# Kernel tuning notes

Hardware: AMD Instinct MI355X
Metric: run time of the kernel (lower is better)

## Reference

```python
import jax, jax.numpy as jnp
import numpy as np

N, E, H, L, T, NH = 20000, 200000, 128, 10, 2, 4


def _ln(x, g, b, eps=1e-5):
    mu = jnp.mean(x, -1, keepdims=True)
    d = x - mu
    v = jnp.mean(d * d, -1, keepdims=True)
    return d * jax.lax.rsqrt(v + eps) * g + b


def _mha(q_in, kv_in, wqkv, bqkv, wo, bo, nh=NH):
    # torch nn.MultiheadAttention (batch=1, eval mode)
    Hd = q_in.shape[-1]
    d = Hd // nh
    wq, wk, wv = jnp.split(wqkv, 3, axis=1)
    bq, bk, bv = jnp.split(bqkv, 3)
    q = (q_in @ wq + bq).reshape(-1, nh, d)
    k = (kv_in @ wk + bk).reshape(-1, nh, d)
    v = (kv_in @ wv + bv).reshape(-1, nh, d)
    s = jnp.einsum('qhd,khd->hqk', q, k) / jnp.sqrt(jnp.float32(d))
    a = jax.nn.softmax(s, axis=-1)
    o = jnp.einsum('hqk,khd->qhd', a, v).reshape(-1, Hd)
    return o @ wo + bo


def setup_inputs() -> dict:
    key = jax.random.key(0)
    ks = iter(jax.random.split(key, 64))
    def rn(shape, scale=1.0):
        return jax.random.normal(next(ks), shape, jnp.float32) * scale
    s = 0.05
    inp = {}
    inp['x'] = rn((N, H))
    inp['edge_index'] = jax.random.randint(next(ks), (2, E), 0, N)
    inp['edge_attr'] = rn((E, H))
    # per-layer edge MLP: Linear(3H,2H) LN GELU Linear(2H,H) LN
    inp['edge_w1'] = rn((L, 3 * H, 2 * H), s); inp['edge_b1'] = jnp.zeros((L, 2 * H))
    inp['edge_ln1g'] = jnp.ones((L, 2 * H)); inp['edge_ln1b'] = jnp.zeros((L, 2 * H))
    inp['edge_w2'] = rn((L, 2 * H, H), s); inp['edge_b2'] = jnp.zeros((L, H))
    inp['edge_ln2g'] = jnp.ones((L, H)); inp['edge_ln2b'] = jnp.zeros((L, H))
    # per-layer node MLP: Linear(3H,2H) LN GELU Linear(2H,H) LN
    inp['node_w1'] = rn((L, 3 * H, 2 * H), s); inp['node_b1'] = jnp.zeros((L, 2 * H))
    inp['node_ln1g'] = jnp.ones((L, 2 * H)); inp['node_ln1b'] = jnp.zeros((L, 2 * H))
    inp['node_w2'] = rn((L, 2 * H, H), s); inp['node_b2'] = jnp.zeros((L, H))
    inp['node_ln2g'] = jnp.ones((L, H)); inp['node_ln2b'] = jnp.zeros((L, H))
    # GlobalTokenTransformer (shared across layers)
    inp['token_embed'] = rn((T, H), 0.02)
    inp['tok_wqkv'] = rn((H, 3 * H), s); inp['tok_bqkv'] = jnp.zeros(3 * H)
    inp['tok_wo'] = rn((H, H), s); inp['tok_bo'] = jnp.zeros(H)
    inp['ln_t1g'] = jnp.ones(H); inp['ln_t1b'] = jnp.zeros(H)
    inp['ln_t2g'] = jnp.ones(H); inp['ln_t2b'] = jnp.zeros(H)
    inp['ff_w1'] = rn((H, 4 * H), s); inp['ff_b1'] = jnp.zeros(4 * H)
    inp['ff_w2'] = rn((4 * H, H), s); inp['ff_b2'] = jnp.zeros(H)
    inp['nod_wqkv'] = rn((H, 3 * H), s); inp['nod_bqkv'] = jnp.zeros(3 * H)
    inp['nod_wo'] = rn((H, H), s); inp['nod_bo'] = jnp.zeros(H)
    return inp


def reference(x, edge_index, edge_attr,
              edge_w1, edge_b1, edge_ln1g, edge_ln1b, edge_w2, edge_b2, edge_ln2g, edge_ln2b,
              node_w1, node_b1, node_ln1g, node_ln1b, node_w2, node_b2, node_ln2g, node_ln2b,
              token_embed, tok_wqkv, tok_bqkv, tok_wo, tok_bo,
              ln_t1g, ln_t1b, ln_t2g, ln_t2b, ff_w1, ff_b1, ff_w2, ff_b2,
              nod_wqkv, nod_bqkv, nod_wo, nod_bo):
    row, col = edge_index[0], edge_index[1]
    n = x.shape[0]
    e = edge_index.shape[1]
    # in-degree counts for scatter-mean (identical every layer)
    deg = jnp.clip(jax.ops.segment_sum(jnp.ones((e,), x.dtype), col, num_segments=n), 1.0)[:, None]

    def global_ctx(nodes):
        tokens = token_embed  # [T, H]
        t = _mha(tokens, nodes, tok_wqkv, tok_bqkv, tok_wo, tok_bo)
        tokens = _ln(tokens + t, ln_t1g, ln_t1b)
        ff = jax.nn.gelu(tokens @ ff_w1 + ff_b1, approximate=False) @ ff_w2 + ff_b2
        tokens = _ln(tokens + ff, ln_t2g, ln_t2b)
        return _mha(nodes, tokens, nod_wqkv, nod_bqkv, nod_wo, nod_bo)  # [N, H]

    for i in range(L):
        # edge update: gather -> MLP -> residual
        ei = jnp.concatenate([x[row], x[col], edge_attr], axis=1)  # [E, 3H]
        h = jax.nn.gelu(_ln(ei @ edge_w1[i] + edge_b1[i], edge_ln1g[i], edge_ln1b[i]), approximate=False)
        edge_attr = edge_attr + _ln(h @ edge_w2[i] + edge_b2[i], edge_ln2g[i], edge_ln2b[i])
        # scatter-mean aggregation at destination nodes
        agg = jax.ops.segment_sum(edge_attr, col, num_segments=n) / deg
        ctx = global_ctx(x)
        ni = jnp.concatenate([x, agg, ctx], axis=1)  # [N, 3H]
        h = jax.nn.gelu(_ln(ni @ node_w1[i] + node_b1[i], node_ln1g[i], node_ln1b[i]), approximate=False)
        x = x + _ln(h @ node_w2[i] + node_b2[i], node_ln2g[i], node_ln2b[i])
    return (x, edge_attr)
```

## Files before the change

kernel.cpp:

```cpp
#include <hip/hip_runtime.h>
#include <math.h>

#define Nn 20000
#define Ee 200000
#define Hh 128
#define Ll 10

using short8  = __attribute__((ext_vector_type(8))) short;
using floatx4 = __attribute__((ext_vector_type(4))) float;

__device__ __forceinline__ float bf2f(unsigned short u){ return __uint_as_float(((unsigned)u)<<16); }
__device__ __forceinline__ unsigned short f2bf(float f){
  unsigned u = __float_as_uint(f);
  u += 0x7FFF + ((u>>16)&1);
  return (unsigned short)(u>>16);
}
__device__ __forceinline__ float gelu_f(float x){
  float x3 = x*x*x;
  float z = 1.595769122f*x + 0.071354816f*x3;
  return x / (1.0f + __expf(-z));
}

template<bool GATHER>
__global__ __launch_bounds__(256, 2)
void mlp_fused(const unsigned short* __restrict__ s0,
               const unsigned short* __restrict__ s1,
               const unsigned short* __restrict__ s2b,
               const float* __restrict__ s2f,
               const int* __restrict__ rowI, const int* __restrict__ colI,
               const unsigned short* __restrict__ w1p,
               const unsigned short* __restrict__ w2p,
               const float* __restrict__ pb1, const float* __restrict__ pg1,
               const float* __restrict__ pbb1,
               const float* __restrict__ pb2, const float* __restrict__ pg2,
               const float* __restrict__ pbb2,
               float* __restrict__ resf,
               unsigned short* __restrict__ resb,
               int M)
{
  __shared__ __align__(16) unsigned short wbuf[2][8192];
  __shared__ __align__(16) unsigned short lds_h[4][16*264];
  __shared__ float lds_par[1152];

  const int tid = threadIdx.x;
  const int w = tid>>6, lane = tid&63, l16 = lane&15, q = lane>>4;
  const int R0 = blockIdx.x*64;

  for (int u = tid; u < 1152; u += 256){
    float v;
    if      (u <  256) v = pb1[u];
    else if (u <  512) v = pg1[u-256];
    else if (u <  768) v = pbb1[u-512];
    else if (u <  896) v = pb2[u-768];
    else if (u < 1024) v = pg2[u-896];
    else               v = pbb2[u-1024];
    lds_par[u] = v;
  }

  {
    const unsigned short* src = w1p;
    #pragma unroll
    for (int i=0;i<4;++i)
      *(short8*)&wbuf[0][tid*8 + i*2048] = *(const short8*)(src + tid*8 + i*2048);
  }

  const int gA = R0 + w*16 + l16;

  short8 af[12];
  if (GATHER){
    const unsigned short* p0 = s0 + (size_t)rowI[gA]*Hh + q*8;
    const unsigned short* p1 = s1 + (size_t)colI[gA]*Hh + q*8;
    const float*          p2 = s2f + (size_t)gA*Hh + q*8;
    #pragma unroll
    for (int c=0;c<4;++c){
      af[c]   = *(const short8*)(p0 + c*32);
      af[4+c] = *(const short8*)(p1 + c*32);
      float4 u0 = *(const float4*)(p2 + c*32);
      float4 u1 = *(const float4*)(p2 + c*32 + 4);
      short8 t8;
      t8[0]=(short)f2bf(u0.x); t8[1]=(short)f2bf(u0.y);
      t8[2]=(short)f2bf(u0.z); t8[3]=(short)f2bf(u0.w);
      t8[4]=(short)f2bf(u1.x); t8[5]=(short)f2bf(u1.y);
      t8[6]=(short)f2bf(u1.z); t8[7]=(short)f2bf(u1.w);
      af[8+c] = t8;
    }
  } else {
    int gg = gA < M ? gA : (M-1);
    const unsigned short* p0 = s0 + (size_t)gg*Hh + q*8;
    const unsigned short* p1 = s1 + (size_t)gg*Hh + q*8;
    const unsigned short* p2 = s2b + (size_t)gg*Hh + q*8;
    #pragma unroll
    for (int c=0;c<4;++c){
      af[c]   = *(const short8*)(p0 + c*32);
      af[4+c] = *(const short8*)(p1 + c*32);
      af[8+c] = *(const short8*)(p2 + c*32);
    }
  }

  __syncthreads();

  const floatx4 fz = {0.f,0.f,0.f,0.f};
  floatx4 acc1[16];
  #pragma unroll
  for (int t=0;t<16;++t) acc1[t] = fz;

  #pragma unroll
  for (int c=0;c<12;++c){
    const int sel = c&1, nsel = (c+1)&1;
    short8 nx0, nx1, nx2, nx3;
    if (c < 11){
      const unsigned short* src = w1p + (size_t)(c+1)*8192;
      nx0 = *(const short8*)(src + tid*8);
      nx1 = *(const short8*)(src + tid*8 + 2048);
      nx2 = *(const short8*)(src + tid*8 + 4096);
      nx3 = *(const short8*)(src + tid*8 + 6144);
    } else {
      const unsigned short* src = w2p;
      nx0 = *(const short8*)(src + tid*8);
      nx1 = *(const short8*)(src + tid*8 + 2048);
    }
    #pragma unroll
    for (int t=0;t<16;++t){
      short8 bf = *(const short8*)&wbuf[sel][t*512 + lane*8];
      acc1[t] = __builtin_amdgcn_mfma_f32_16x16x32_bf16(af[c], bf, acc1[t], 0,0,0);
    }
    if (c < 11){
      *(short8*)&wbuf[nsel][tid*8]        = nx0;
      *(short8*)&wbuf[nsel][tid*8 + 2048] = nx1;
      *(short8*)&wbuf[nsel][tid*8 + 4096] = nx2;
      *(short8*)&wbuf[nsel][tid*8 + 6144] = nx3;
    } else {
      *(short8*)&wbuf[0][tid*8]        = nx0;
      *(short8*)&wbuf[0][tid*8 + 2048] = nx1;
    }
    __syncthreads();
  }

  #pragma unroll
  for (int r=0;r<4;++r){
    float hv[16];
    float s=0.f, ss=0.f;
    #pragma unroll
    for (int t=0;t<16;++t){
      float v = acc1[t][r] + lds_par[t*16+l16];
      hv[t]=v; s+=v; ss+=v*v;
    }
    #pragma unroll
    for (int m=1;m<16;m<<=1){ s += __shfl_xor(s,m); ss += __shfl_xor(ss,m); }
    float mean = s*(1.f/256.f);
    float var  = ss*(1.f/256.f) - mean*mean;
    float rstd = rsqrtf(var + 1e-5f);
    int ro = q*4 + r;
    #pragma unroll
    for (int t=0;t<16;++t){
      int col = t*16+l16;
      float hh = (hv[t]-mean)*rstd*lds_par[256+col] + lds_par[512+col];
      lds_h[w][ro*264 + col] = f2bf(gelu_f(hh));
    }
  }

  floatx4 acc2[8];
  #pragma unroll
  for (int t=0;t<8;++t) acc2[t] = fz;

  #pragma unroll
  for (int c=0;c<8;++c){
    const int sel = c&1, nsel = (c+1)&1;
    short8 nx0, nx1;
    if (c < 7){
      const unsigned short* src = w2p + (size_t)(c+1)*4096;
      nx0 = *(const short8*)(src + tid*8);
      nx1 = *(const short8*)(src + tid*8 + 2048);
    }
    short8 a2 = *(const short8*)&lds_h[w][l16*264 + c*32 + q*8];
    #pragma unroll
    for (int t=0;t<8;++t){
      short8 bf = *(const short8*)&wbuf[sel][t*512 + lane*8];
      acc2[t] = __builtin_amdgcn_mfma_f32_16x16x32_bf16(a2, bf, acc2[t], 0,0,0);
    }
    if (c < 7){
      *(short8*)&wbuf[nsel][tid*8]        = nx0;
      *(short8*)&wbuf[nsel][tid*8 + 2048] = nx1;
    }
    __syncthreads();
  }

  #pragma unroll
  for (int r=0;r<4;++r){
    float vv[8];
    float s=0.f, ss=0.f;
    #pragma unroll
    for (int t=0;t<8;++t){
      float v = acc2[t][r] + lds_par[768 + t*16+l16];
      vv[t]=v; s+=v; ss+=v*v;
    }
    #pragma unroll
    for (int m=1;m<16;m<<=1){ s += __shfl_xor(s,m); ss += __shfl_xor(ss,m); }
    float mean = s*(1.f/128.f);
    float var  = ss*(1.f/128.f) - mean*mean;
    float rstd = rsqrtf(var + 1e-5f);
    int g = R0 + w*16 + q*4 + r;
    if (g < M){
      #pragma unroll
      for (int t=0;t<8;++t){
        int col = t*16+l16;
        float outv = (vv[t]-mean)*rstd*lds_par[896+col] + lds_par[1024+col];
        size_t idx = (size_t)g*Hh + col;
        float nv = resf[idx] + outv;
        resf[idx] = nv;
        if (!GATHER) resb[idx] = f2bf(nv);
      }
    }
  }
}

__global__ void csr_prefix(const int* __restrict__ cnt, int* __restrict__ rowPtr)
{
  __shared__ int part[256];
  const int tid = threadIdx.x;
  const int CH = (Nn + 255)/256;
  int c0 = tid*CH; if (c0 > Nn) c0 = Nn;
  int c1 = c0+CH;  if (c1 > Nn) c1 = Nn;
  int s = 0;
  for (int i=c0;i<c1;++i) s += cnt[i];
  part[tid] = s;
  __syncthreads();
  for (int d=1; d<256; d<<=1){
    int v = (tid>=d) ? part[tid-d] : 0;
    __syncthreads();
    part[tid] += v;
    __syncthreads();
  }
  int off = part[tid] - s;
  for (int i=c0;i<c1;++i){ rowPtr[i] = off; off += cnt[i]; }
  if (tid == 255) rowPtr[Nn] = off;
}

__global__ void csr_fill(const int* __restrict__ colI, const int* __restrict__ rowPtr,
                         int* __restrict__ cursor, int* __restrict__ elist)
{
  int e = blockIdx.x*256 + threadIdx.x;
  if (e < Ee){
    int n = colI[e];
    int p = atomicAdd(&cursor[n], 1);
    elist[rowPtr[n] + p] = e;
  }
}

__global__ __launch_bounds__(256, 8)
void agg_gather(const float* __restrict__ ef, const int* __restrict__ rowPtr,
                const int* __restrict__ elist, const float* __restrict__ invd,
                unsigned short* __restrict__ aggb)
{
  int n = blockIdx.x*4 + (threadIdx.x>>6);
  int lane = threadIdx.x & 63;
  if (n >= Nn) return;
  int j0 = rowPtr[n], j1 = rowPtr[n+1];
  float s0=0.f, s1=0.f, t0=0.f, t1=0.f;
  int j = j0;
  for (; j+1 < j1; j += 2){
    int e0 = elist[j], e1 = elist[j+1];
    float2 a = *(const float2*)(ef + (size_t)e0*Hh + lane*2);
    float2 b = *(const float2*)(ef + (size_t)e1*Hh + lane*2);
    s0 += a.x; s1 += a.y; t0 += b.x; t1 += b.y;
  }
  if (j < j1){
    int e0 = elist[j];
    float2 a = *(const float2*)(ef + (size_t)e0*Hh + lane*2);
    s0 += a.x; s1 += a.y;
  }
  s0 += t0; s1 += t1;
  float iv = invd[n];
  unsigned int packed = ((unsigned)f2bf(s1*iv) << 16) | (unsigned)f2bf(s0*iv);
  *(unsigned int*)&aggb[(size_t)n*Hh + lane*2] = packed;
}

template<int NCOLS>
__global__ __launch_bounds__(256, 4)
void gemm_bias(const unsigned short* __restrict__ A,
               const unsigned short* __restrict__ Wp,
               const float* __restrict__ bias,
               unsigned short* __restrict__ out,
               int M)
{
  constexpr int NT = NCOLS/16;
  const int tid = threadIdx.x;
  const int w = tid>>6, lane = tid&63, l16 = lane&15, q = lane>>4;
  const int R0 = blockIdx.x*64;
  int gA = R0 + w*16 + l16;
  int ga = gA < M ? gA : (M-1);
  const unsigned short* ap = A + (size_t)ga*128 + q*8;

  const floatx4 fz = {0.f,0.f,0.f,0.f};
  floatx4 acc[NT];
  #pragma unroll
  for (int t=0;t<NT;++t) acc[t] = fz;

  const unsigned short* wl = Wp + (size_t)lane*8;
  #pragma unroll
  for (int c=0;c<4;++c){
    short8 af = *(const short8*)(ap + c*32);
    #pragma unroll
    for (int t=0;t<NT;++t){
      short8 bf = *(const short8*)(wl + (size_t)(c*NT+t)*512);
      acc[t] = __builtin_amdgcn_mfma_f32_16x16x32_bf16(af, bf, acc[t], 0,0,0);
    }
  }
  #pragma unroll
  for (int r=0;r<4;++r){
    int g = R0 + w*16 + q*4 + r;
    if (g < M){
      #pragma unroll
      for (int t=0;t<NT;++t){
        int col = t*16+l16;
        out[(size_t)g*NCOLS + col] = f2bf(acc[t][r] + bias[col]);
      }
    }
  }
}

__global__ __launch_bounds__(256, 2)
void attn_reduce(const unsigned short* __restrict__ kv, const float* __restrict__ tq,
                 float* __restrict__ onum, float* __restrict__ denom, int Nv)
{
  __shared__ float sbuf[8][256];
  __shared__ float qs[256];
  int tid = threadIdx.x;
  qs[tid] = tq[tid];
  __syncthreads();
  int base = blockIdx.x*256;
  int i = base + tid;
  float ex[8];
  if (i < Nv){
    const unsigned short* kr = kv + (size_t)i*256;
    float acc[8];
    #pragma unroll
    for (int a=0;a<8;++a) acc[a]=0.f;
    #pragma unroll
    for (int d8=0; d8<16; ++d8){
      short8 k8 = *(const short8*)(kr + d8*8);
      #pragma unroll
      for (int u=0;u<8;++u){
        int d = d8*8+u;
        float kd = bf2f((unsigned short)k8[u]);
        int h = d>>5;
        acc[h]   += qs[d]*kd;
        acc[4+h] += qs[128+d]*kd;
      }
    }
    #pragma unroll
    for (int a=0;a<8;++a) ex[a] = expf(acc[a]*0.17677669529663688f);
  } else {
    #pragma unroll
    for (int a=0;a<8;++a) ex[a]=0.f;
  }
  #pragma unroll
  for (int a=0;a<8;++a) sbuf[a][tid] = ex[a];
  __syncthreads();
  int th = tid>>5, d = tid&31, h = th&3;
  int cnt = Nv - base; if (cnt > 256) cnt = 256;
  float accv = 0.f, dsum = 0.f;
  #pragma unroll 4
  for (int j=0;j<cnt;++j){
    float wgt = sbuf[th][j];
    accv += wgt * bf2f(kv[(size_t)(base+j)*256 + 128 + h*32 + d]);
    dsum += wgt;
  }
  atomicAdd(&onum[th*32+d], accv);
  if (d==0) atomicAdd(&denom[th], dsum);
}

__global__ void token_kernel(const float* __restrict__ onum, const float* __restrict__ denom,
  const float* __restrict__ tok_wo, const float* __restrict__ tok_bo,
  const float* __restrict__ token_embed,
  const float* __restrict__ g1, const float* __restrict__ b1,
  const float* __restrict__ g2, const float* __restrict__ b2,
  const float* __restrict__ ff_w1, const float* __restrict__ ff_b1,
  const float* __restrict__ ff_w2, const float* __restrict__ ff_b2,
  const float* __restrict__ nod_wqkv, const float* __restrict__ nod_bqkv,
  float* __restrict__ kv2)
{
  __shared__ float O[2][128];
  __shared__ float T[2][128];
  __shared__ float F[2][512];
  __shared__ float stats[4];
  int tid = threadIdx.x;
  int t = tid>>7, c = tid&127;
  {
    int th = t*4 + (c>>5);
    O[t][c] = onum[th*32 + (c&31)] / denom[th];
  }
  __syncthreads();
  {
    float s = tok_bo[c];
    for (int k=0;k<128;++k) s += O[t][k]*tok_wo[k*128+c];
    T[t][c] = token_embed[t*128+c] + s;
  }
  __syncthreads();
  if (tid < 2){
    float s=0.f, ss=0.f;
    for (int k=0;k<128;++k){ float v=T[tid][k]; s+=v; ss+=v*v; }
    float m = s*(1.f/128.f);
    stats[tid*2] = m;
    stats[tid*2+1] = rsqrtf(ss*(1.f/128.f)-m*m+1e-5f);
  }
  __syncthreads();
  T[t][c] = (T[t][c]-stats[t*2])*stats[t*2+1]*g1[c] + b1[c];
  __syncthreads();
  for (int u=0;u<4;++u){
    int o = tid + u*256;
    int tt = o>>9, j = o&511;
    float s = ff_b1[j];
    for (int k=0;k<128;++k) s += T[tt][k]*ff_w1[k*512+j];
    F[tt][j] = gelu_f(s);
  }
  __syncthreads();
  {
    float s = ff_b2[c];
    for (int k=0;k<512;++k) s += F[t][k]*ff_w2[k*128+c];
    O[t][c] = T[t][c] + s;
  }
  __syncthreads();
  if (tid < 2){
    float s=0.f, ss=0.f;
    for (int k=0;k<128;++k){ float v=O[tid][k]; s+=v; ss+=v*v; }
    float m = s*(1.f/128.f);
    stats[tid*2] = m;
    stats[tid*2+1] = rsqrtf(ss*(1.f/128.f)-m*m+1e-5f);
  }
  __syncthreads();
  O[t][c] = (O[t][c]-stats[t*2])*stats[t*2+1]*g2[c] + b2[c];
  __syncthreads();
  for (int u=0;u<2;++u){
    int o = tid + u*256;
    int tt = o>>8, cc = o&255;
    float s = nod_bqkv[128+cc];
    for (int k=0;k<128;++k) s += O[tt][k]*nod_wqkv[k*384+128+cc];
    if (cc < 128) kv2[tt*128+cc] = s;
    else          kv2[256 + tt*128 + (cc-128)] = s;
  }
}

__global__ void node_attn(const unsigned short* __restrict__ qn,
                          const float* __restrict__ kv2,
                          unsigned short* __restrict__ attn, int Nv)
{
  __shared__ float k2s[256], v2s[256];
  int tid = threadIdx.x;
  k2s[tid] = kv2[tid];
  v2s[tid] = kv2[256+tid];
  __syncthreads();
  int g = blockIdx.x*8 + (tid>>5);
  int d = tid&31;
  int i = g>>2, h = g&3;
  if (i >= Nv) return;
  int c = h*32+d;
  float qv = bf2f(qn[(size_t)i*128 + c]);
  float p0 = qv * k2s[c];
  float p1 = qv * k2s[128+c];
  #pragma unroll
  for (int m=1;m<32;m<<=1){ p0 += __shfl_xor(p0,m); p1 += __shfl_xor(p1,m); }
  float e0 = expf(p0*0.17677669529663688f);
  float e1 = expf(p1*0.17677669529663688f);
  float outv = (e0*v2s[c] + e1*v2s[128+c]) / (e0+e1);
  attn[(size_t)i*128 + c] = f2bf(outv);
}

__global__ void prep_weights(const float* __restrict__ ew1,
  const float* __restrict__ ew2,
  const float* __restrict__ nw1,
  const float* __restrict__ nw2,
  const float* __restrict__ tok_wqkv,
  const float* __restrict__ nod_wqkv,
  const float* __restrict__ nod_wo,
  const float* __restrict__ token_embed,
  const float* __restrict__ tok_bqkv,
  unsigned short* __restrict__ ew1p, unsigned short* __restrict__ ew2p,
  unsigned short* __restrict__ nw1p, unsigned short* __restrict__ nw2p,
  unsigned short* __restrict__ kvp, unsigned short* __restrict__ qnp,
  unsigned short* __restrict__ wop, float* __restrict__ tq)
{
  int gid = blockIdx.x*256 + threadIdx.x;
  if (gid < Ll*98304){
    int l = gid / 98304; int idx = gid % 98304;
    int c = idx >> 13;
    int t = (idx >> 9) & 15;
    int lane = (idx >> 3) & 63;
    int j = idx & 7;
    int k = c*32 + (lane>>4)*8 + j;
    int n = t*16 + (lane&15);
    size_t src = (size_t)l*98304 + (size_t)k*256 + n;
    ew1p[gid] = f2bf(ew1[src]);
    nw1p[gid] = f2bf(nw1[src]);
  }
  if (gid < Ll*32768){
    int l = gid / 32768; int idx = gid % 32768;
    int c = idx >> 12;
    int t = (idx >> 9) & 7;
    int lane = (idx >> 3) & 63;
    int j = idx & 7;
    int k = c*32 + (lane>>4)*8 + j;
    int n = t*16 + (lane&15);
    size_t src = (size_t)l*32768 + (size_t)k*128 + n;
    ew2p[gid] = f2bf(ew2[src]);
    nw2p[gid] = f2bf(nw2[src]);
  }
  if (gid < 32768){
    int c = gid >> 13;
    int t = (gid >> 9) & 15;
    int lane = (gid >> 3) & 63;
    int j = gid & 7;
    int k = c*32 + (lane>>4)*8 + j;
    int n = t*16 + (lane&15);
    kvp[gid] = f2bf(tok_wqkv[(size_t)k*384 + 128 + n]);
  }
  if (gid < 16384){
    int c = gid >> 12;
    int t = (gid >> 9) & 7;
    int lane = (gid >> 3) & 63;
    int j = gid & 7;
    int k = c*32 + (lane>>4)*8 + j;
    int n = t*16 + (lane&15);
    qnp[gid] = f2bf(nod_wqkv[(size_t)k*384 + n]);
    wop[gid] = f2bf(nod_wo[(size_t)k*128 + n]);
  }
  if (gid < 256){
    int t = gid >> 7, c = gid & 127;
    float s = tok_bqkv[c];
    for (int k=0;k<128;++k) s += token_embed[t*128+k] * tok_wqkv[k*384+c];
    tq[gid] = s;
  }
}

__global__ void init_state(const float* __restrict__ x_in,
  const float* __restrict__ e_in,
  float* __restrict__ x_f32, float* __restrict__ e_f32,
  unsigned short* __restrict__ x_b16)
{
  size_t gid = (size_t)blockIdx.x*256 + threadIdx.x;
  if (gid < (size_t)Ee*Hh) e_f32[gid] = e_in[gid];
  if (gid < (size_t)Nn*Hh){
    float v = x_in[gid];
    x_f32[gid] = v;
    x_b16[gid] = f2bf(v);
  }
}

__global__ void deg_count(const int* __restrict__ colI, int* __restrict__ cnt){
  int gid = blockIdx.x*256+threadIdx.x;
  if (gid < Ee) atomicAdd(&cnt[colI[gid]], 1);
}
__global__ void deg_inv(const int* __restrict__ cnt, float* __restrict__ inv){
  int gid = blockIdx.x*256+threadIdx.x;
  if (gid < Nn){ int c = cnt[gid]; inv[gid] = 1.0f / (float)(c > 1 ? c : 1); }
}

extern "C" void kernel_launch(void* const* d_in, const int* in_sizes, int n_in,
                              void* d_out, int out_size, void* d_ws, size_t ws_size,
                              hipStream_t stream)
{
  const float* x_in       = (const float*)d_in[0];
  const int*   eidx       = (const int*)d_in[1];
  const float* e_in       = (const float*)d_in[2];
  const float* edge_w1    = (const float*)d_in[3];
  const float* edge_b1    = (const float*)d_in[4];
  const float* edge_ln1g  = (const float*)d_in[5];
  const float* edge_ln1b  = (const float*)d_in[6];
  const float* edge_w2    = (const float*)d_in[7];
  const float* edge_b2    = (const float*)d_in[8];
  const float* edge_ln2g  = (const float*)d_in[9];
  const float* edge_ln2b  = (const float*)d_in[10];
  const float* node_w1    = (const float*)d_in[11];
  const float* node_b1    = (const float*)d_in[12];
  const float* node_ln1g  = (const float*)d_in[13];
  const float* node_ln1b  = (const float*)d_in[14];
  const float* node_w2    = (const float*)d_in[15];
  const float* node_b2    = (const float*)d_in[16];
  const float* node_ln2g  = (const float*)d_in[17];
  const float* node_ln2b  = (const float*)d_in[18];
  const float* token_embed= (const float*)d_in[19];
  const float* tok_wqkv   = (const float*)d_in[20];
  const float* tok_bqkv   = (const float*)d_in[21];
  const float* tok_wo     = (const float*)d_in[22];
  const float* tok_bo     = (const float*)d_in[23];
  const float* ln_t1g     = (const float*)d_in[24];
  const float* ln_t1b     = (const float*)d_in[25];
  const float* ln_t2g     = (const float*)d_in[26];
  const float* ln_t2b     = (const float*)d_in[27];
  const float* ff_w1      = (const float*)d_in[28];
  const float* ff_b1      = (const float*)d_in[29];
  const float* ff_w2      = (const float*)d_in[30];
  const float* ff_b2      = (const float*)d_in[31];
  const float* nod_wqkv   = (const float*)d_in[32];
  const float* nod_bqkv   = (const float*)d_in[33];
  const float* nod_wo     = (const float*)d_in[34];
  const float* nod_bo     = (const float*)d_in[35];

  const int* rowI = eidx;
  const int* colI = eidx + Ee;

  float* out_x = (float*)d_out;
  float* out_e = out_x + (size_t)Nn*Hh;

  char* base = (char*)d_ws;
  size_t off = 0;
  auto alloc = [&](size_t bytes)->char*{
    char* p = base + off; off += (bytes + 255) & ~(size_t)255; return p;
  };
  unsigned short* x_b16 = (unsigned short*)alloc((size_t)Nn*Hh*2);
  unsigned short* agg_b = (unsigned short*)alloc((size_t)Nn*Hh*2);
  unsigned short* ctx_b = (unsigned short*)alloc((size_t)Nn*Hh*2);
  unsigned short* kv_b  = (unsigned short*)alloc((size_t)Nn*256*2);
  unsigned short* qn_b  = (unsigned short*)alloc((size_t)Nn*Hh*2);
  unsigned short* at_b  = (unsigned short*)alloc((size_t)Nn*Hh*2);
  float*          invd  = (float*)alloc((size_t)Nn*4);
  int*            dcnt  = (int*)alloc((size_t)Nn*4);
  int*            rowP  = (int*)alloc((size_t)(Nn+1)*4);
  int*            curs  = (int*)alloc((size_t)Nn*4);
  int*            elist = (int*)alloc((size_t)Ee*4);
  unsigned short* ew1p  = (unsigned short*)alloc((size_t)Ll*98304*2);
  unsigned short* ew2p  = (unsigned short*)alloc((size_t)Ll*32768*2);
  unsigned short* nw1p  = (unsigned short*)alloc((size_t)Ll*98304*2);
  unsigned short* nw2p  = (unsigned short*)alloc((size_t)Ll*32768*2);
  unsigned short* kvp   = (unsigned short*)alloc((size_t)32768*2);
  unsigned short* qnp   = (unsigned short*)alloc((size_t)16384*2);
  unsigned short* wop   = (unsigned short*)alloc((size_t)16384*2);
  float*          tq    = (float*)alloc(256*4);
  float*          kv2   = (float*)alloc(512*4);
  float*          onum  = (float*)alloc(264*4);
  float*          denom = onum + 256;
  if (off > ws_size) return;

  hipMemsetAsync(dcnt, 0, (size_t)Nn*4, stream);
  hipMemsetAsync(curs, 0, (size_t)Nn*4, stream);
  prep_weights<<<(Ll*98304 + 255)/256, 256, 0, stream>>>(
      edge_w1, edge_w2, node_w1, node_w2, tok_wqkv, nod_wqkv, nod_wo,
      token_embed, tok_bqkv, ew1p, ew2p, nw1p, nw2p, kvp, qnp, wop, tq);
  init_state<<<(int)(((size_t)Ee*Hh + 255)/256), 256, 0, stream>>>(
      x_in, e_in, out_x, out_e, x_b16);
  deg_count<<<(Ee+255)/256, 256, 0, stream>>>(colI, dcnt);
  csr_prefix<<<1, 256, 0, stream>>>(dcnt, rowP);
  deg_inv<<<(Nn+255)/256, 256, 0, stream>>>(dcnt, invd);
  csr_fill<<<(Ee+255)/256, 256, 0, stream>>>(colI, rowP, curs, elist);

  for (int l = 0; l < Ll; ++l){
    hipMemsetAsync(onum, 0, 264*4, stream);

    mlp_fused<true><<<Ee/64, 256, 0, stream>>>(x_b16, x_b16, nullptr, out_e,
        rowI, colI,
        ew1p + (size_t)l*98304, ew2p + (size_t)l*32768,
        edge_b1 + l*256, edge_ln1g + l*256, edge_ln1b + l*256,
        edge_b2 + l*128, edge_ln2g + l*128, edge_ln2b + l*128,
        out_e, nullptr, Ee);
    agg_gather<<<(Nn+3)/4, 256, 0, stream>>>(out_e, rowP, elist, invd, agg_b);

    gemm_bias<256><<<(Nn+63)/64, 256, 0, stream>>>(x_b16, kvp, tok_bqkv+128, kv_b, Nn);
    attn_reduce<<<(Nn+255)/256, 256, 0, stream>>>(kv_b, tq, onum, denom, Nn);
    token_kernel<<<1, 256, 0, stream>>>(onum, denom, tok_wo, tok_bo, token_embed,
        ln_t1g, ln_t1b, ln_t2g, ln_t2b, ff_w1, ff_b1, ff_w2, ff_b2,
        nod_wqkv, nod_bqkv, kv2);
    gemm_bias<128><<<(Nn+63)/64, 256, 0, stream>>>(x_b16, qnp, nod_bqkv, qn_b, Nn);
    node_attn<<<(Nn*4 + 7)/8, 256, 0, stream>>>(qn_b, kv2, at_b, Nn);
    gemm_bias<128><<<(Nn+63)/64, 256, 0, stream>>>(at_b, wop, nod_bo, ctx_b, Nn);

    mlp_fused<false><<<(Nn+63)/64, 256, 0, stream>>>(x_b16, agg_b, ctx_b, nullptr,
        nullptr, nullptr,
        nw1p + (size_t)l*98304, nw2p + (size_t)l*32768,
        node_b1 + l*256, node_ln1g + l*256, node_ln1b + l*256,
        node_b2 + l*128, node_ln2g + l*128, node_ln2b + l*128,
        out_x, x_b16, Nn);
  }
}
```

Before: 3.526 ms.

## Merge per-layer kernels into horizontally fused launches and fuse attention with Wo GEMM

Packs the KV and Q projections together with the edge MLP into one launch, chosen by block index, and does the same for scatter-mean aggregation and the attention reduction. Node attention is fused into the output-projection GEMM, so the at_b intermediate buffer goes away. The second MLP stage now reads W2 straight from global/L2 instead of double-buffering it through LDS with barriers. This cuts launch count and intermediate traffic and lets independent work share the GPU, at the cost of block-type imbalance and possibly uncoalesced global weight reads in the MLP.

```diff
diff --git a/kernel.cpp b/kernel.cpp
--- a/kernel.cpp
+++ b/kernel.cpp
@@ -5,6 +5,11 @@
 #define Ee 200000
 #define Hh 128
 #define Ll 10
+
+#define NB_PROJ 313
+#define NB_EDGE (Ee/64)
+#define NB_AGG  (Nn/4)
+#define NB_ATTN ((Nn+255)/256)
 
 using short8  = __attribute__((ext_vector_type(8))) short;
 using floatx4 = __attribute__((ext_vector_type(4))) float;
@@ -22,8 +27,8 @@
 }
 
 template<bool GATHER>
-__global__ __launch_bounds__(256, 2)
-void mlp_fused(const unsigned short* __restrict__ s0,
+__device__ __forceinline__ void mlp_body(int bid,
+               const unsigned short* __restrict__ s0,
                const unsigned short* __restrict__ s1,
                const unsigned short* __restrict__ s2b,
                const float* __restrict__ s2f,
@@ -44,7 +49,7 @@
 
   const int tid = threadIdx.x;
   const int w = tid>>6, lane = tid&63, l16 = lane&15, q = lane>>4;
-  const int R0 = blockIdx.x*64;
+  const int R0 = bid*64;
 
   for (int u = tid; u < 1152; u += 256){
     float v;
@@ -106,7 +111,7 @@
 
   #pragma unroll
   for (int c=0;c<12;++c){
-    const int sel = c&1, nsel = (c+1)&1;
+    const int sel = c&1, nsel = sel^1;
     short8 nx0, nx1, nx2, nx3;
     if (c < 11){
       const unsigned short* src = w1p + (size_t)(c+1)*8192;
@@ -114,10 +119,6 @@
       nx1 = *(const short8*)(src + tid*8 + 2048);
       nx2 = *(const short8*)(src + tid*8 + 4096);
       nx3 = *(const short8*)(src + tid*8 + 6144);
-    } else {
-      const unsigned short* src = w2p;
-      nx0 = *(const short8*)(src + tid*8);
-      nx1 = *(const short8*)(src + tid*8 + 2048);
     }
     #pragma unroll
     for (int t=0;t<16;++t){
@@ -129,11 +130,8 @@
       *(short8*)&wbuf[nsel][tid*8 + 2048] = nx1;
       *(short8*)&wbuf[nsel][tid*8 + 4096] = nx2;
       *(short8*)&wbuf[nsel][tid*8 + 6144] = nx3;
-    } else {
-      *(short8*)&wbuf[0][tid*8]        = nx0;
-      *(short8*)&wbuf[0][tid*8 + 2048] = nx1;
-    }
-    __syncthreads();
+      __syncthreads();
+    }
   }
 
   #pragma unroll
@@ -163,26 +161,15 @@
   #pragma unroll
   for (int t=0;t<8;++t) acc2[t] = fz;
 
+  const unsigned short* w2l = w2p + (size_t)lane*8;
   #pragma unroll
   for (int c=0;c<8;++c){
-    const int sel = c&1, nsel = (c+1)&1;
-    short8 nx0, nx1;
-    if (c < 7){
-      const unsigned short* src = w2p + (size_t)(c+1)*4096;
-      nx0 = *(const short8*)(src + tid*8);
-      nx1 = *(const short8*)(src + tid*8 + 2048);
-    }
     short8 a2 = *(const short8*)&lds_h[w][l16*264 + c*32 + q*8];
     #pragma unroll
     for (int t=0;t<8;++t){
-      short8 bf = *(const short8*)&wbuf[sel][t*512 + lane*8];
+      short8 bf = *(const short8*)(w2l + (size_t)(c*8+t)*512);
       acc2[t] = __builtin_amdgcn_mfma_f32_16x16x32_bf16(a2, bf, acc2[t], 0,0,0);
     }
-    if (c < 7){
-      *(short8*)&wbuf[nsel][tid*8]        = nx0;
-      *(short8*)&wbuf[nsel][tid*8 + 2048] = nx1;
-    }
-    __syncthreads();
   }
 
   #pragma unroll
@@ -214,70 +201,9 @@
   }
 }
 
-__global__ void csr_prefix(const int* __restrict__ cnt, int* __restrict__ rowPtr)
-{
-  __shared__ int part[256];
-  const int tid = threadIdx.x;
-  const int CH = (Nn + 255)/256;
-  int c0 = tid*CH; if (c0 > Nn) c0 = Nn;
-  int c1 = c0+CH;  if (c1 > Nn) c1 = Nn;
-  int s = 0;
-  for (int i=c0;i<c1;++i) s += cnt[i];
-  part[tid] = s;
-  __syncthreads();
-  for (int d=1; d<256; d<<=1){
-    int v = (tid>=d) ? part[tid-d] : 0;
-    __syncthreads();
-    part[tid] += v;
-    __syncthreads();
-  }
-  int off = part[tid] - s;
-  for (int i=c0;i<c1;++i){ rowPtr[i] = off; off += cnt[i]; }
-  if (tid == 255) rowPtr[Nn] = off;
-}
-
-__global__ void csr_fill(const int* __restrict__ colI, const int* __restrict__ rowPtr,
-                         int* __restrict__ cursor, int* __restrict__ elist)
-{
-  int e = blockIdx.x*256 + threadIdx.x;
-  if (e < Ee){
-    int n = colI[e];
-    int p = atomicAdd(&cursor[n], 1);
-    elist[rowPtr[n] + p] = e;
-  }
-}
-
-__global__ __launch_bounds__(256, 8)
-void agg_gather(const float* __restrict__ ef, const int* __restrict__ rowPtr,
-                const int* __restrict__ elist, const float* __restrict__ invd,
-                unsigned short* __restrict__ aggb)
-{
-  int n = blockIdx.x*4 + (threadIdx.x>>6);
-  int lane = threadIdx.x & 63;
-  if (n >= Nn) return;
-  int j0 = rowPtr[n], j1 = rowPtr[n+1];
-  float s0=0.f, s1=0.f, t0=0.f, t1=0.f;
-  int j = j0;
-  for (; j+1 < j1; j += 2){
-    int e0 = elist[j], e1 = elist[j+1];
-    float2 a = *(const float2*)(ef + (size_t)e0*Hh + lane*2);
-    float2 b = *(const float2*)(ef + (size_t)e1*Hh + lane*2);
-    s0 += a.x; s1 += a.y; t0 += b.x; t1 += b.y;
-  }
-  if (j < j1){
-    int e0 = elist[j];
-    float2 a = *(const float2*)(ef + (size_t)e0*Hh + lane*2);
-    s0 += a.x; s1 += a.y;
-  }
-  s0 += t0; s1 += t1;
-  float iv = invd[n];
-  unsigned int packed = ((unsigned)f2bf(s1*iv) << 16) | (unsigned)f2bf(s0*iv);
-  *(unsigned int*)&aggb[(size_t)n*Hh + lane*2] = packed;
-}
-
 template<int NCOLS>
-__global__ __launch_bounds__(256, 4)
-void gemm_bias(const unsigned short* __restrict__ A,
+__device__ __forceinline__ void proj_body(int bid,
+               const unsigned short* __restrict__ A,
                const unsigned short* __restrict__ Wp,
                const float* __restrict__ bias,
                unsigned short* __restrict__ out,
@@ -286,7 +212,7 @@
   constexpr int NT = NCOLS/16;
   const int tid = threadIdx.x;
   const int w = tid>>6, lane = tid&63, l16 = lane&15, q = lane>>4;
-  const int R0 = blockIdx.x*64;
+  const int R0 = bid*64;
   int gA = R0 + w*16 + l16;
   int ga = gA < M ? gA : (M-1);
   const unsigned short* ap = A + (size_t)ga*128 + q*8;
@@ -320,18 +246,98 @@
 }
 
 __global__ __launch_bounds__(256, 2)
-void attn_reduce(const unsigned short* __restrict__ kv, const float* __restrict__ tq,
-                 float* __restrict__ onum, float* __restrict__ denom, int Nv)
-{
+void mega_edge(const unsigned short* __restrict__ xb,
+               const float* __restrict__ ef,
+               const int* __restrict__ rowI, const int* __restrict__ colI,
+               const unsigned short* __restrict__ w1p,
+               const unsigned short* __restrict__ w2p,
+               const float* __restrict__ pb1, const float* __restrict__ pg1,
+               const float* __restrict__ pbb1,
+               const float* __restrict__ pb2, const float* __restrict__ pg2,
+               const float* __restrict__ pbb2,
+               float* __restrict__ resf,
+               const unsigned short* __restrict__ kvp, const float* __restrict__ bkv,
+               unsigned short* __restrict__ kvb,
+               const unsigned short* __restrict__ qnp, const float* __restrict__ bqn,
+               unsigned short* __restrict__ qnb)
+{
+  int bid = blockIdx.x;
+  if (bid < NB_PROJ){
+    proj_body<256>(bid, xb, kvp, bkv, kvb, Nn);
+    return;
+  }
+  if (bid < 2*NB_PROJ){
+    proj_body<128>(bid - NB_PROJ, xb, qnp, bqn, qnb, Nn);
+    return;
+  }
+  mlp_body<true>(bid - 2*NB_PROJ, xb, xb, nullptr, ef, rowI, colI,
+                 w1p, w2p, pb1, pg1, pbb1, pb2, pg2, pbb2,
+                 resf, nullptr, Ee);
+}
+
+__global__ __launch_bounds__(256, 2)
+void node_mlp(const unsigned short* __restrict__ xb,
+              const unsigned short* __restrict__ aggb,
+              const unsigned short* __restrict__ ctxb,
+              const unsigned short* __restrict__ w1p,
+              const unsigned short* __restrict__ w2p,
+              const float* __restrict__ pb1, const float* __restrict__ pg1,
+              const float* __restrict__ pbb1,
+              const float* __restrict__ pb2, const float* __restrict__ pg2,
+              const float* __restrict__ pbb2,
+              float* __restrict__ resf,
+              unsigned short* __restrict__ resb)
+{
+  mlp_body<false>(blockIdx.x, xb, aggb, ctxb, nullptr, nullptr, nullptr,
+                  w1p, w2p, pb1, pg1, pbb1, pb2, pg2, pbb2,
+                  resf, resb, Nn);
+}
+
+__global__ __launch_bounds__(256, 4)
+void mega2(const float* __restrict__ ef, const int* __restrict__ rowPtr,
+           const int* __restrict__ elist, const float* __restrict__ invd,
+           unsigned short* __restrict__ aggb,
+           const unsigned short* __restrict__ kv, const float* __restrict__ tq,
+           float* __restrict__ onum, float* __restrict__ denom)
+{
+  const int bid = blockIdx.x;
+  const int tid = threadIdx.x;
+
+  if (bid < NB_AGG){
+    int n = bid*4 + (tid>>6);
+    int lane = tid&63;
+    if (n >= Nn) return;
+    int j0 = rowPtr[n], j1 = rowPtr[n+1];
+    float s0=0.f,s1=0.f,t0=0.f,t1=0.f,u0=0.f,u1=0.f,v0=0.f,v1=0.f;
+    int j = j0;
+    for (; j+3 < j1; j += 4){
+      int e0=elist[j], e1=elist[j+1], e2=elist[j+2], e3=elist[j+3];
+      float2 a = *(const float2*)(ef + (size_t)e0*Hh + lane*2);
+      float2 b = *(const float2*)(ef + (size_t)e1*Hh + lane*2);
+      float2 c = *(const float2*)(ef + (size_t)e2*Hh + lane*2);
+      float2 d = *(const float2*)(ef + (size_t)e3*Hh + lane*2);
+      s0+=a.x; s1+=a.y; t0+=b.x; t1+=b.y; u0+=c.x; u1+=c.y; v0+=d.x; v1+=d.y;
+    }
+    for (; j < j1; ++j){
+      int e0 = elist[j];
+      float2 a = *(const float2*)(ef + (size_t)e0*Hh + lane*2);
+      s0+=a.x; s1+=a.y;
+    }
+    s0 += t0+u0+v0; s1 += t1+u1+v1;
+    float iv = invd[n];
+    unsigned int packed = ((unsigned)f2bf(s1*iv) << 16) | (unsigned)f2bf(s0*iv);
+    *(unsigned int*)&aggb[(size_t)n*Hh + lane*2] = packed;
+    return;
+  }
+
   __shared__ float sbuf[8][256];
   __shared__ float qs[256];
-  int tid = threadIdx.x;
   qs[tid] = tq[tid];
   __syncthreads();
-  int base = blockIdx.x*256;
-  int i = base + tid;
+  const int base = (bid - NB_AGG)*256;
+  const int i = base + tid;
   float ex[8];
-  if (i < Nv){
+  if (i < Nn){
     const unsigned short* kr = kv + (size_t)i*256;
     float acc[8];
     #pragma unroll
@@ -357,17 +363,22 @@
   #pragma unroll
   for (int a=0;a<8;++a) sbuf[a][tid] = ex[a];
   __syncthreads();
-  int th = tid>>5, d = tid&31, h = th&3;
-  int cnt = Nv - base; if (cnt > 256) cnt = 256;
-  float accv = 0.f, dsum = 0.f;
-  #pragma unroll 4
-  for (int j=0;j<cnt;++j){
-    float wgt = sbuf[th][j];
-    accv += wgt * bf2f(kv[(size_t)(base+j)*256 + 128 + h*32 + d]);
-    dsum += wgt;
-  }
-  atomicAdd(&onum[th*32+d], accv);
-  if (d==0) atomicAdd(&denom[th], dsum);
+
+  const int jh = tid>>7, h = (tid>>5)&3, d = tid&31;
+  int cnt = Nn - base; if (cnt > 256) cnt = 256;
+  int j0 = jh*128, j1 = j0+128;
+  if (j0 > cnt) j0 = cnt;
+  if (j1 > cnt) j1 = cnt;
+  float a0=0.f, a1=0.f, w0s=0.f, w1s=0.f;
+  for (int j=j0; j<j1; ++j){
+    float w0 = sbuf[h][j];
+    float w1 = sbuf[4+h][j];
+    float vv = bf2f(kv[(size_t)(base+j)*256 + 128 + h*32 + d]);
+    a0 += w0*vv; a1 += w1*vv; w0s += w0; w1s += w1;
+  }
+  atomicAdd(&onum[h*32+d], a0);
+  atomicAdd(&onum[128+h*32+d], a1);
+  if (d==0){ atomicAdd(&denom[h], w0s); atomicAdd(&denom[4+h], w1s); }
 }
 
 __global__ void token_kernel(const float* __restrict__ onum, const float* __restrict__ denom,
@@ -441,29 +452,104 @@
   }
 }
 
-__global__ void node_attn(const unsigned short* __restrict__ qn,
-                          const float* __restrict__ kv2,
-                          unsigned short* __restrict__ attn, int Nv)
+__global__ __launch_bounds__(256, 4)
+void attn_wo_gemm(const unsigned short* __restrict__ qn,
+                  const float* __restrict__ kv2,
+                  const unsigned short* __restrict__ wop,
+                  const float* __restrict__ nod_bo,
+                  unsigned short* __restrict__ out,
+                  int M)
 {
   __shared__ float k2s[256], v2s[256];
-  int tid = threadIdx.x;
+  const int tid = threadIdx.x;
   k2s[tid] = kv2[tid];
   v2s[tid] = kv2[256+tid];
   __syncthreads();
-  int g = blockIdx.x*8 + (tid>>5);
-  int d = tid&31;
-  int i = g>>2, h = g&3;
-  if (i >= Nv) return;
-  int c = h*32+d;
-  float qv = bf2f(qn[(size_t)i*128 + c]);
-  float p0 = qv * k2s[c];
-  float p1 = qv * k2s[128+c];
-  #pragma unroll
-  for (int m=1;m<32;m<<=1){ p0 += __shfl_xor(p0,m); p1 += __shfl_xor(p1,m); }
-  float e0 = expf(p0*0.17677669529663688f);
-  float e1 = expf(p1*0.17677669529663688f);
-  float outv = (e0*v2s[c] + e1*v2s[128+c]) / (e0+e1);
-  attn[(size_t)i*128 + c] = f2bf(outv);
+  const int w = tid>>6, lane = tid&63, l16 = lane&15, q = lane>>4;
+  const int R0 = blockIdx.x*64;
+  int gA = R0 + w*16 + l16;
+  int ga = gA < M ? gA : (M-1);
+  const unsigned short* ap = qn + (size_t)ga*128 + q*8;
+
+  const floatx4 fz = {0.f,0.f,0.f,0.f};
+  floatx4 acc[8];
+  #pragma unroll
+  for (int t=0;t<8;++t) acc[t] = fz;
+  const unsigned short* wl = wop + (size_t)lane*8;
+
+  #pragma unroll
+  for (int c=0;c<4;++c){
+    short8 qv8 = *(const short8*)(ap + c*32);
+    float qv[8];
+    float p0=0.f, p1=0.f;
+    #pragma unroll
+    for (int j=0;j<8;++j){
+      qv[j] = bf2f((unsigned short)qv8[j]);
+      int col = c*32 + q*8 + j;
+      p0 += qv[j]*k2s[col];
+      p1 += qv[j]*k2s[128+col];
+    }
+    p0 += __shfl_xor(p0,16); p0 += __shfl_xor(p0,32);
+    p1 += __shfl_xor(p1,16); p1 += __shfl_xor(p1,32);
+    float e0 = __expf(p0*0.17677669529663688f);
+    float e1 = __expf(p1*0.17677669529663688f);
+    float inv = 1.0f/(e0+e1);
+    short8 a;
+    #pragma unroll
+    for (int j=0;j<8;++j){
+      int col = c*32 + q*8 + j;
+      a[j] = (short)f2bf((e0*v2s[col] + e1*v2s[128+col])*inv);
+    }
+    #pragma unroll
+    for (int t=0;t<8;++t){
+      short8 bf = *(const short8*)(wl + (size_t)(c*8+t)*512);
+      acc[t] = __builtin_amdgcn_mfma_f32_16x16x32_bf16(a, bf, acc[t], 0,0,0);
+    }
+  }
+  #pragma unroll
+  for (int r=0;r<4;++r){
+    int g = R0 + w*16 + q*4 + r;
+    if (g < M){
+      #pragma unroll
+      for (int t=0;t<8;++t){
+        int col = t*16+l16;
+        out[(size_t)g*128 + col] = f2bf(acc[t][r] + nod_bo[col]);
+      }
+    }
+  }
+}
+
+__global__ void csr_prefix(const int* __restrict__ cnt, int* __restrict__ rowPtr)
+{
+  __shared__ int part[256];
+  const int tid = threadIdx.x;
+  const int CH = (Nn + 255)/256;
+  int c0 = tid*CH; if (c0 > Nn) c0 = Nn;
+  int c1 = c0+CH;  if (c1 > Nn) c1 = Nn;
+  int s = 0;
+  for (int i=c0;i<c1;++i) s += cnt[i];
+  part[tid] = s;
+  __syncthreads();
+  for (int d=1; d<256; d<<=1){
+    int v = (tid>=d) ? part[tid-d] : 0;
+    __syncthreads();
+    part[tid] += v;
+    __syncthreads();
+  }
+  int off = part[tid] - s;
+  for (int i=c0;i<c1;++i){ rowPtr[i] = off; off += cnt[i]; }
+  if (tid == 255) rowPtr[Nn] = off;
+}
+
+__global__ void csr_fill(const int* __restrict__ colI, const int* __restrict__ rowPtr,
+                         int* __restrict__ cursor, int* __restrict__ elist)
+{
+  int e = blockIdx.x*256 + threadIdx.x;
+  if (e < Ee){
+    int n = colI[e];
+    int p = atomicAdd(&cursor[n], 1);
+    elist[rowPtr[n] + p] = e;
+  }
 }
 
 __global__ void prep_weights(const float* __restrict__ ew1,
@@ -612,7 +698,6 @@
   unsigned short* ctx_b = (unsigned short*)alloc((size_t)Nn*Hh*2);
   unsigned short* kv_b  = (unsigned short*)alloc((size_t)Nn*256*2);
   unsigned short* qn_b  = (unsigned short*)alloc((size_t)Nn*Hh*2);
-  unsigned short* at_b  = (unsigned short*)alloc((size_t)Nn*Hh*2);
   float*          invd  = (float*)alloc((size_t)Nn*4);
   int*            dcnt  = (int*)alloc((size_t)Nn*4);
   int*            rowP  = (int*)alloc((size_t)(Nn+1)*4);
@@ -646,28 +731,28 @@
   for (int l = 0; l < Ll; ++l){
     hipMemsetAsync(onum, 0, 264*4, stream);
 
-    mlp_fused<true><<<Ee/64, 256, 0, stream>>>(x_b16, x_b16, nullptr, out_e,
-        rowI, colI,
+    mega_edge<<<2*NB_PROJ + NB_EDGE, 256, 0, stream>>>(
+        x_b16, out_e, rowI, colI,
         ew1p + (size_t)l*98304, ew2p + (size_t)l*32768,
         edge_b1 + l*256, edge_ln1g + l*256, edge_ln1b + l*256,
         edge_b2 + l*128, edge_ln2g + l*128, edge_ln2b + l*128,
-        out_e, nullptr, Ee);
-    agg_gather<<<(Nn+3)/4, 256, 0, stream>>>(out_e, rowP, elist, invd, agg_b);
-
-    gemm_bias<256><<<(Nn+63)/64, 256, 0, stream>>>(x_b16, kvp, tok_bqkv+128, kv_b, Nn);
-    attn_reduce<<<(Nn+255)/256, 256, 0, stream>>>(kv_b, tq, onum, denom, Nn);
+        out_e,
+        kvp, tok_bqkv+128, kv_b,
+        qnp, nod_bqkv, qn_b);
+
+    mega2<<<NB_AGG + NB_ATTN, 256, 0, stream>>>(
+        out_e, rowP, elist, invd, agg_b, kv_b, tq, onum, denom);
+
     token_kernel<<<1, 256, 0, stream>>>(onum, denom, tok_wo, tok_bo, token_embed,
         ln_t1g, ln_t1b, ln_t2g, ln_t2b, ff_w1, ff_b1, ff_w2, ff_b2,
         nod_wqkv, nod_bqkv, kv2);
-    gemm_bias<128><<<(Nn+63)/64, 256, 0, stream>>>(x_b16, qnp, nod_bqkv, qn_b, Nn);
-    node_attn<<<(Nn*4 + 7)/8, 256, 0, stream>>>(qn_b, kv2, at_b, Nn);
-    gemm_bias<128><<<(Nn+63)/64, 256, 0, stream>>>(at_b, wop, nod_bo, ctx_b, Nn);
-
-    mlp_fused<false><<<(Nn+63)/64, 256, 0, stream>>>(x_b16, agg_b, ctx_b, nullptr,
-        nullptr, nullptr,
+
+    attn_wo_gemm<<<NB_PROJ, 256, 0, stream>>>(qn_b, kv2, wop, nod_bo, ctx_b, Nn);
+
+    node_mlp<<<NB_PROJ, 256, 0, stream>>>(x_b16, agg_b, ctx_b,
         nw1p + (size_t)l*98304, nw2p + (size_t)l*32768,
         node_b1 + l*256, node_ln1g + l*256, node_ln1b + l*256,
         node_b2 + l*128, node_ln2g + l*128, node_ln2b + l*128,
-        out_x, x_b16, Nn);
-  }
-}
+        out_x, x_b16);
+  }
+}
```

Result: slower. 3.662 ms (+3.9%).
